# Kernel tuning notes

Measured on AMD Instinct MI355X. Metric: run time of the kernel, lower is better.

Reference implementation:

```python
import jax, jax.numpy as jnp
import numpy as np
from jax import lax

H, MEM, AUX = 1024, 256, 16
S = MEM + AUX          # total_slots
B, T = 8, 4096
TOPK = 8               # top_k_binding
GAMMA, BETA, PTS = 0.92, 0.08, 0.4  # gamma, beta, prediction_torque_scale
RANK = 10              # coupling_rank == prediction_rank


def _inv_softplus(v):
    return float(np.log(np.expm1(max(float(v), 1e-6))))


def setup_inputs() -> dict:
    key = jax.random.key(0)
    ks = jax.random.split(key, 8)
    x = jax.random.normal(ks[0], (B, T, H), dtype=jnp.float32)
    # base basis: orthonormal columns in the first MEM slots (memory_dim < hidden_dim -> QR branch)
    q, _ = jnp.linalg.qr(jax.random.normal(ks[1], (H, MEM), dtype=jnp.float32))
    basis = jnp.zeros((H, S), jnp.float32).at[:, :MEM].set(q)
    return dict(
        x=x,
        basis=basis,
        tape_init_re=jax.random.normal(ks[2], (S,), dtype=jnp.float32) / S ** 0.5,
        tape_init_im=jax.random.normal(ks[3], (S,), dtype=jnp.float32) / S ** 0.5,
        eta_raw=jnp.asarray(_inv_softplus(0.08), jnp.float32),
        alpha=jnp.asarray(0.35, jnp.float32),
        torque_rotation=jnp.zeros((S,), jnp.float32),
        w_r=jnp.zeros((S,), jnp.float32),
        breadth_gate=jnp.zeros((S,), jnp.float32),
        epsilon_factor=jax.random.normal(ks[4], (S, RANK), dtype=jnp.float32) * 0.02,
        epsilon_scale=jnp.zeros((RANK,), jnp.float32),
        epsilon_diag=jnp.zeros((S,), jnp.float32),
        pred_factor=jax.random.normal(ks[5], (S, RANK), dtype=jnp.float32) * 0.02,
        pred_scale=jnp.zeros((RANK,), jnp.float32),
        pred_diag=jnp.zeros((S,), jnp.float32),
    )


def _forward(x, basis, tape_init_re, tape_init_im, eta_raw, alpha,
             torque_rotation, w_r, breadth_gate,
             epsilon_factor, epsilon_scale, epsilon_diag,
             pred_factor, pred_scale, pred_diag):
    active = jnp.arange(S) < MEM                      # base slots active (fixed population)
    amf = active.astype(jnp.float32)
    eta = jax.nn.softplus(eta_raw)
    # low-rank Hermitian coupling epsilon and prediction operator W_pred
    eps = (epsilon_factor * epsilon_scale) @ epsilon_factor.T + jnp.diag(epsilon_diag)
    wp = (pred_factor * pred_scale) @ pred_factor.T + jnp.diag(pred_diag)
    eps_c = eps.astype(jnp.complex64)
    wp_c = wp.astype(jnp.complex64)
    rot = jnp.exp(1j * torque_rotation.astype(jnp.complex64))  # torque phase rotation
    wr_gate = jax.nn.sigmoid(w_r)
    bg = jax.nn.sigmoid(breadth_gate)

    def renorm(tape):
        masked = tape * amf
        nrm = jnp.sqrt(jnp.maximum((jnp.abs(masked) ** 2).sum(-1, keepdims=True), 1e-16))
        return masked / nrm

    tape0 = (tape_init_re + 1j * tape_init_im) * amf   # aux slots zeroed as in _complex_tape_init
    tape0 = renorm(jnp.broadcast_to(tape0, (B, S)))

    def step(carry, x_t):
        tape, prev = carry                              # [B,S] complex64 each
        m = jnp.einsum('hs,bh->bs', basis, x_t)         # project into slot space
        mag = jnp.abs(m) * amf
        kth = lax.top_k(mag, TOPK)[0][:, -1:]           # top-k binding threshold
        inj = jnp.where((mag >= kth) & active, m, 0.0).astype(jnp.complex64)
        rotated = tape * rot
        drive = jnp.einsum('st,bt->bs', eps_c, rotated)  # coupling drive
        pred = jnp.einsum('st,bt->bs', wp_c, rotated)    # prediction torque
        new = (GAMMA * rotated + eta * drive + BETA * inj
               + PTS * 1j * pred + wr_gate * prev)
        new = renorm(new)
        y = x_t + alpha * jnp.einsum('hs,bs->bh', basis, bg * new.real)
        return (new, tape), y

    (_, _), ys = lax.scan(step, (tape0, tape0), jnp.swapaxes(x, 0, 1))
    return jnp.swapaxes(ys, 0, 1)


def reference(x, basis, tape_init_re, tape_init_im, eta_raw, alpha,
              torque_rotation, w_r, breadth_gate,
              epsilon_factor, epsilon_scale, epsilon_diag,
              pred_factor, pred_scale, pred_diag):
    return _forward(x, basis, tape_init_re, tape_init_im, eta_raw, alpha,
                    torque_rotation, w_r, breadth_gate,
                    epsilon_factor, epsilon_scale, epsilon_diag,
                    pred_factor, pred_scale, pred_diag)
```

## Files before the change

kernel.cpp:

```cpp
#include <hip/hip_runtime.h>
#include <cstdint>
#include <cstddef>

#define HD    1024
#define SLOTS 272
#define MEMS  256
#define BATCH 8
#define TT    4096
#define RR    (BATCH*TT)
#define RANKC 10

#define GAMMA 0.92f
#define BETA  0.08f
#define PTS   0.4f

typedef float f32x2 __attribute__((ext_vector_type(2)));
#define PKFMA(a, b, c) __builtin_elementwise_fma((a), (b), (c))

#define DPP_ADD(v, ctrl, rmask)                                                   \
    v += __int_as_float(__builtin_amdgcn_update_dpp(                              \
        0, __float_as_int(v), (ctrl), (rmask), 0xf, true))

__device__ __forceinline__ float wave_sum_bcast(float v)
{
    DPP_ADD(v, 0xB1,  0xf);
    DPP_ADD(v, 0x4E,  0xf);
    DPP_ADD(v, 0x141, 0xf);
    DPP_ADD(v, 0x140, 0xf);
    DPP_ADD(v, 0x142, 0xa);
    DPP_ADD(v, 0x143, 0xc);
    return __int_as_float(__builtin_amdgcn_readlane(__float_as_int(v), 63));
}

__global__ void prep_kernel(const float* __restrict__ t0re, const float* __restrict__ t0im,
                            const float* __restrict__ eta_raw,
                            const float* __restrict__ trot, const float* __restrict__ w_r,
                            const float* __restrict__ bgate,
                            const float* __restrict__ eps_scale, const float* __restrict__ pred_scale,
                            const float* __restrict__ eps_diag, const float* __restrict__ pred_diag,
                            float* __restrict__ consts, int* __restrict__ flags)
{
    __shared__ float red[MEMS];
    const int s = threadIdx.x;
    const float tr = t0re[s], ti = t0im[s];
    red[s] = tr * tr + ti * ti;
    __syncthreads();
    for (int off = 128; off > 0; off >>= 1) {
        if (s < off) red[s] += red[s + off];
        __syncthreads();
    }
    const float nrm = sqrtf(fmaxf(red[0], 1e-16f));
    const float eta = log1pf(expf(eta_raw[0]));
    const float rc = cosf(trot[s]), rs = sinf(trot[s]);
    const float c1 = GAMMA + eta * eps_diag[s];
    const float c2 = PTS * pred_diag[s];
    consts[0 * MEMS + s] = 1.0f / (1.0f + expf(-w_r[s]));
    consts[1 * MEMS + s] = 1.0f / (1.0f + expf(-bgate[s]));
    consts[2 * MEMS + s] = c1 * rc - c2 * rs;
    consts[3 * MEMS + s] = c1 * rs + c2 * rc;
    consts[4 * MEMS + s] = tr / nrm;
    consts[5 * MEMS + s] = ti / nrm;
    consts[6 * MEMS + s] = rc;
    consts[7 * MEMS + s] = rs;
    if (s == 0) {
        consts[8 * MEMS] = eta;
        int f1 = 0, f2 = 0;
        for (int k = 0; k < RANKC; ++k) {
            if (eps_scale[k]  != 0.0f) f1 = 1;
            if (pred_scale[k] != 0.0f) f2 = 1;
        }
        flags[0] = f1;
        flags[1] = f2;
    }
}

__global__ __launch_bounds__(256) void proj_kernel(const float* __restrict__ x,
                                                   const float* __restrict__ basis,
                                                   float* __restrict__ M)
{
    __shared__ float As[32][68];
    __shared__ float Bs[32][68];
    const int tid  = threadIdx.x;
    const int row0 = blockIdx.x * 64;
    const int col0 = blockIdx.y * 64;
    const int mt = tid >> 4, nt = tid & 15;
    float acc[4][4] = {};
    for (int k0 = 0; k0 < HD; k0 += 32) {
        {
            int q = tid, m = q >> 3, kq = q & 7;
            float4 a = *(const float4*)&x[(size_t)(row0 + m) * HD + k0 + kq * 4];
            As[kq * 4 + 0][m] = a.x; As[kq * 4 + 1][m] = a.y;
            As[kq * 4 + 2][m] = a.z; As[kq * 4 + 3][m] = a.w;
            q = tid + 256; m = q >> 3; kq = q & 7;
            float4 b = *(const float4*)&x[(size_t)(row0 + m) * HD + k0 + kq * 4];
            As[kq * 4 + 0][m] = b.x; As[kq * 4 + 1][m] = b.y;
            As[kq * 4 + 2][m] = b.z; As[kq * 4 + 3][m] = b.w;
            q = tid; int k = q >> 4; int nq = q & 15;
            float4 c = *(const float4*)&basis[(size_t)(k0 + k) * SLOTS + col0 + nq * 4];
            *(float4*)&Bs[k][nq * 4] = c;
            q = tid + 256; k = q >> 4; nq = q & 15;
            float4 d = *(const float4*)&basis[(size_t)(k0 + k) * SLOTS + col0 + nq * 4];
            *(float4*)&Bs[k][nq * 4] = d;
        }
        __syncthreads();
#pragma unroll
        for (int kk = 0; kk < 32; ++kk) {
            float4 a = *(const float4*)&As[kk][mt * 4];
            float4 b = *(const float4*)&Bs[kk][nt * 4];
            float av[4] = {a.x, a.y, a.z, a.w};
            float bv[4] = {b.x, b.y, b.z, b.w};
#pragma unroll
            for (int i = 0; i < 4; ++i)
#pragma unroll
                for (int j = 0; j < 4; ++j) acc[i][j] += av[i] * bv[j];
        }
        __syncthreads();
    }
#pragma unroll
    for (int i = 0; i < 4; ++i) {
        float4 o = {acc[i][0], acc[i][1], acc[i][2], acc[i][3]};
        *(float4*)&M[(size_t)(row0 + mt * 4 + i) * MEMS + col0 + nt * 4] = o;
    }
}

__global__ __launch_bounds__(64) void topk_kernel(float* __restrict__ M)
{
    const int r    = blockIdx.x;
    const int lane = threadIdx.x;
    float4 v = *(const float4*)&M[(size_t)r * MEMS + lane * 4];
    float vals[4] = {fabsf(v.x), fabsf(v.y), fabsf(v.z), fabsf(v.w)};
    float keep[4] = {vals[0], vals[1], vals[2], vals[3]};
    float kv = 0.0f;
#pragma unroll
    for (int it = 0; it < 8; ++it) {
        float lm = vals[0]; int li = 0;
#pragma unroll
        for (int j = 1; j < 4; ++j)
            if (vals[j] > lm) { lm = vals[j]; li = j; }
        float bm = lm; int bi = lane * 4 + li;
#pragma unroll
        for (int off = 1; off < 64; off <<= 1) {
            float om = __shfl_xor(bm, off);
            int   oi = __shfl_xor(bi, off);
            if (om > bm || (om == bm && oi < bi)) { bm = om; bi = oi; }
        }
        kv = bm;
        if ((bi >> 2) == lane) vals[bi & 3] = -1.0f;
    }
    float4 o;
    o.x = (keep[0] >= kv) ? BETA * v.x : 0.0f;
    o.y = (keep[1] >= kv) ? BETA * v.y : 0.0f;
    o.z = (keep[2] >= kv) ? BETA * v.z : 0.0f;
    o.w = (keep[3] >= kv) ? BETA * v.w : 0.0f;
    *(float4*)&M[(size_t)r * MEMS + lane * 4] = o;
}

__global__ __launch_bounds__(64) void scan_kernel(const float* __restrict__ M,
                                                  const float* __restrict__ consts,
                                                  const int* __restrict__ flags,
                                                  const float* __restrict__ eps_fac,
                                                  const float* __restrict__ eps_scale,
                                                  const float* __restrict__ eps_diag,
                                                  const float* __restrict__ pred_fac,
                                                  const float* __restrict__ pred_scale,
                                                  const float* __restrict__ pred_diag,
                                                  float* __restrict__ Wout)
{
    const int b    = blockIdx.x;
    const int lane = threadIdx.x;
    const int s0   = lane * 4;
    const int general = flags[0] | flags[1];
    const size_t base = (size_t)b * TT * MEMS + s0;

    if (!general) {
        f32x2 wr2[2], A2[2], B2[2], nB2[2], vr[2], vi[2], qr[2], qi[2];
        {
            const float4 w4 = *(const float4*)&consts[0 * MEMS + s0];
            const float4 a4 = *(const float4*)&consts[2 * MEMS + s0];
            const float4 b4 = *(const float4*)&consts[3 * MEMS + s0];
            const float4 r4 = *(const float4*)&consts[4 * MEMS + s0];
            const float4 i4 = *(const float4*)&consts[5 * MEMS + s0];
            wr2[0] = {w4.x, w4.y};  wr2[1] = {w4.z, w4.w};
            A2[0]  = {a4.x, a4.y};  A2[1]  = {a4.z, a4.w};
            B2[0]  = {b4.x, b4.y};  B2[1]  = {b4.z, b4.w};
            nB2[0] = {-b4.x, -b4.y}; nB2[1] = {-b4.z, -b4.w};
            vr[0]  = {r4.x, r4.y};  vr[1]  = {r4.z, r4.w};
            vi[0]  = {i4.x, i4.y};  vi[1]  = {i4.z, i4.w};
            qr[0] = vr[0]; qr[1] = vr[1];
            qi[0] = vi[0]; qi[1] = vi[1];
        }
        float4 mbuf[16];
#pragma unroll
        for (int j = 0; j < 16; ++j)
            mbuf[j] = *(const float4*)&M[base + (size_t)j * MEMS];
        for (int t0 = 0; t0 < TT; t0 += 16) {
#pragma unroll
            for (int j = 0; j < 16; ++j) {
                const int t = t0 + j;
                const float4 mc = mbuf[j];
                mbuf[j] = *(const float4*)&M[base + (size_t)(t + 16) * MEMS];
                const f32x2 m0 = {mc.x, mc.y};
                const f32x2 m1 = {mc.z, mc.w};
                const f32x2 u1r0 = PKFMA(A2[0], vr[0], PKFMA(nB2[0], vi[0], PKFMA(wr2[0], qr[0], m0)));
                const f32x2 u1i0 = PKFMA(B2[0], vr[0], PKFMA(A2[0], vi[0], wr2[0] * qi[0]));
                const f32x2 u1r1 = PKFMA(A2[1], vr[1], PKFMA(nB2[1], vi[1], PKFMA(wr2[1], qr[1], m1)));
                const f32x2 u1i1 = PKFMA(B2[1], vr[1], PKFMA(A2[1], vi[1], wr2[1] * qi[1]));
                const f32x2 ps0 = PKFMA(u1i0, u1i0, u1r0 * u1r0);
                const f32x2 ps1 = PKFMA(u1i1, u1i1, u1r1 * u1r1);
                const f32x2 pp  = ps0 + ps1;
                float ss = pp.x + pp.y;
                ss = wave_sum_bcast(ss);
                const float invn = __builtin_amdgcn_rsqf(fmaxf(ss, 1e-16f));
                const f32x2 inv2 = {invn, invn};
                const f32x2 nvr0 = u1r0 * inv2, nvi0 = u1i0 * inv2;
                const f32x2 nvr1 = u1r1 * inv2, nvi1 = u1i1 * inv2;
                const float4 wq = {nvr0.x, nvr0.y, nvr1.x, nvr1.y};
                *(float4*)&Wout[base + (size_t)t * MEMS] = wq;
                qr[0] = vr[0]; qi[0] = vi[0];
                qr[1] = vr[1]; qi[1] = vi[1];
                vr[0] = nvr0;  vi[0] = nvi0;
                vr[1] = nvr1;  vi[1] = nvi1;
            }
        }
        return;
    }

    float wr4[4], ur[4], ui[4], pr[4], pi[4];
    float rc4[4], rs4[4], ed4[4], pd4[4];
#pragma unroll
    for (int i = 0; i < 4; ++i) {
        wr4[i] = consts[0 * MEMS + s0 + i];
        ur[i]  = consts[4 * MEMS + s0 + i];
        ui[i]  = consts[5 * MEMS + s0 + i];
        pr[i] = ur[i]; pi[i] = ui[i];
        rc4[i] = consts[6 * MEMS + s0 + i];
        rs4[i] = consts[7 * MEMS + s0 + i];
        ed4[i] = eps_diag[s0 + i];
        pd4[i] = pred_diag[s0 + i];
    }
    const float eta  = consts[8 * MEMS];
    const int es_any = flags[0];
    const int ps_any = flags[1];
    float4 mbuf[4];
#pragma unroll
    for (int j = 0; j < 4; ++j)
        mbuf[j] = *(const float4*)&M[base + (size_t)j * MEMS];
    for (int t0 = 0; t0 < TT; t0 += 4) {
#pragma unroll
        for (int j = 0; j < 4; ++j) {
            const int t = t0 + j;
            const float4 mc = mbuf[j];
            mbuf[j] = *(const float4*)&M[base + (size_t)(t + 4) * MEMS];
            float rr[4], ri[4], nr[4], ni[4];
#pragma unroll
            for (int i = 0; i < 4; ++i) {
                rr[i] = ur[i] * rc4[i] - ui[i] * rs4[i];
                ri[i] = ur[i] * rs4[i] + ui[i] * rc4[i];
            }
            const float mv[4] = {mc.x, mc.y, mc.z, mc.w};
#pragma unroll
            for (int i = 0; i < 4; ++i) {
                nr[i] = GAMMA * rr[i] + wr4[i] * pr[i] + eta * ed4[i] * rr[i]
                        - PTS * pd4[i] * ri[i] + mv[i];
                ni[i] = GAMMA * ri[i] + wr4[i] * pi[i] + eta * ed4[i] * ri[i]
                        + PTS * pd4[i] * rr[i];
            }
            if (es_any) {
#pragma unroll
                for (int k = 0; k < RANKC; ++k) {
                    float u[4], prj = 0.0f, pij = 0.0f;
#pragma unroll
                    for (int i = 0; i < 4; ++i) {
                        u[i] = eps_fac[(size_t)(s0 + i) * RANKC + k];
                        prj = fmaf(u[i], rr[i], prj);
                        pij = fmaf(u[i], ri[i], pij);
                    }
                    prj = wave_sum_bcast(prj);
                    pij = wave_sum_bcast(pij);
                    const float sc = eta * eps_scale[k];
#pragma unroll
                    for (int i = 0; i < 4; ++i) {
                        nr[i] = fmaf(sc * u[i], prj, nr[i]);
                        ni[i] = fmaf(sc * u[i], pij, ni[i]);
                    }
                }
            }
            if (ps_any) {
#pragma unroll
                for (int k = 0; k < RANKC; ++k) {
                    float u[4], qrj = 0.0f, qij = 0.0f;
#pragma unroll
                    for (int i = 0; i < 4; ++i) {
                        u[i] = pred_fac[(size_t)(s0 + i) * RANKC + k];
                        qrj = fmaf(u[i], rr[i], qrj);
                        qij = fmaf(u[i], ri[i], qij);
                    }
                    qrj = wave_sum_bcast(qrj);
                    qij = wave_sum_bcast(qij);
                    const float sc = PTS * pred_scale[k];
#pragma unroll
                    for (int i = 0; i < 4; ++i) {
                        nr[i] = fmaf(-sc * u[i], qij, nr[i]);
                        ni[i] = fmaf( sc * u[i], qrj, ni[i]);
                    }
                }
            }
            float ss = 0.0f;
#pragma unroll
            for (int i = 0; i < 4; ++i) ss = fmaf(nr[i], nr[i], fmaf(ni[i], ni[i], ss));
            ss = wave_sum_bcast(ss);
            const float inv = __builtin_amdgcn_rsqf(fmaxf(ss, 1e-16f));
#pragma unroll
            for (int i = 0; i < 4; ++i) {
                pr[i] = ur[i]; pi[i] = ui[i];
                ur[i] = nr[i] * inv; ui[i] = ni[i] * inv;
            }
            const float4 wq = {ur[0], ur[1], ur[2], ur[3]};
            *(float4*)&Wout[base + (size_t)t * MEMS] = wq;
        }
    }
}

__global__ __launch_bounds__(256) void outp_kernel(const float* __restrict__ W,
                                                   const float* __restrict__ basis,
                                                   const float* __restrict__ x,
                                                   const float* __restrict__ alpha_p,
                                                   const float* __restrict__ consts,
                                                   float* __restrict__ y)
{
    __shared__ float As[32][68];
    __shared__ float Bs[32][68];
    const int tid  = threadIdx.x;
    const int row0 = blockIdx.x * 64;
    const int col0 = blockIdx.y * 64;
    const int mt = tid >> 4, nt = tid & 15;
    const float alpha = alpha_p[0];
    const float* bgc  = consts + MEMS;
    const int m0 = tid >> 3, m1 = (tid + 256) >> 3;
    const int kq0 = tid & 7;
    float acc[4][4] = {};
    for (int k0 = 0; k0 < MEMS; k0 += 32) {
        {
            const float4 bgv = *(const float4*)&bgc[k0 + kq0 * 4];
            const float bx = alpha * bgv.x, by = alpha * bgv.y;
            const float bz = alpha * bgv.z, bw = alpha * bgv.w;
            float4 a = *(const float4*)&W[(size_t)(row0 + m0) * MEMS + k0 + kq0 * 4];
            As[kq0 * 4 + 0][m0] = a.x; As[kq0 * 4 + 1][m0] = a.y;
            As[kq0 * 4 + 2][m0] = a.z; As[kq0 * 4 + 3][m0] = a.w;
            float4 b = *(const float4*)&W[(size_t)(row0 + m1) * MEMS + k0 + kq0 * 4];
            As[kq0 * 4 + 0][m1] = b.x; As[kq0 * 4 + 1][m1] = b.y;
            As[kq0 * 4 + 2][m1] = b.z; As[kq0 * 4 + 3][m1] = b.w;
            int q = tid; int n = q >> 3;
            float4 c = *(const float4*)&basis[(size_t)(col0 + n) * SLOTS + k0 + kq0 * 4];
            Bs[kq0 * 4 + 0][n] = c.x * bx; Bs[kq0 * 4 + 1][n] = c.y * by;
            Bs[kq0 * 4 + 2][n] = c.z * bz; Bs[kq0 * 4 + 3][n] = c.w * bw;
            q = tid + 256; n = q >> 3;
            float4 d = *(const float4*)&basis[(size_t)(col0 + n) * SLOTS + k0 + kq0 * 4];
            Bs[kq0 * 4 + 0][n] = d.x * bx; Bs[kq0 * 4 + 1][n] = d.y * by;
            Bs[kq0 * 4 + 2][n] = d.z * bz; Bs[kq0 * 4 + 3][n] = d.w * bw;
        }
        __syncthreads();
#pragma unroll
        for (int kk = 0; kk < 32; ++kk) {
            float4 a = *(const float4*)&As[kk][mt * 4];
            float4 b = *(const float4*)&Bs[kk][nt * 4];
            float av[4] = {a.x, a.y, a.z, a.w};
            float bv[4] = {b.x, b.y, b.z, b.w};
#pragma unroll
            for (int i = 0; i < 4; ++i)
#pragma unroll
                for (int j = 0; j < 4; ++j) acc[i][j] += av[i] * bv[j];
        }
        __syncthreads();
    }
#pragma unroll
    for (int i = 0; i < 4; ++i) {
        const size_t ro = (size_t)(row0 + mt * 4 + i) * HD + col0 + nt * 4;
        float4 xv = *(const float4*)&x[ro];
        float4 o  = {xv.x + acc[i][0], xv.y + acc[i][1],
                     xv.z + acc[i][2], xv.w + acc[i][3]};
        *(float4*)&y[ro] = o;
    }
}

extern "C" void kernel_launch(void* const* d_in, const int* in_sizes, int n_in,
                              void* d_out, int out_size, void* d_ws, size_t ws_size,
                              hipStream_t stream)
{
    const float* x          = (const float*)d_in[0];
    const float* basis      = (const float*)d_in[1];
    const float* t0re       = (const float*)d_in[2];
    const float* t0im       = (const float*)d_in[3];
    const float* eta_raw    = (const float*)d_in[4];
    const float* alpha      = (const float*)d_in[5];
    const float* trot       = (const float*)d_in[6];
    const float* w_r        = (const float*)d_in[7];
    const float* bgate      = (const float*)d_in[8];
    const float* eps_fac    = (const float*)d_in[9];
    const float* eps_scale  = (const float*)d_in[10];
    const float* eps_diag   = (const float*)d_in[11];
    const float* pred_fac   = (const float*)d_in[12];
    const float* pred_scale = (const float*)d_in[13];
    const float* pred_diag  = (const float*)d_in[14];
    float* out = (float*)d_out;

    const size_t szM = (size_t)RR * MEMS * sizeof(float);
    const size_t szW = szM;
    const size_t szC = 16384;

    char* ws = (char*)d_ws;
    float *Mbuf, *Wbuf, *cbuf;
    if (ws_size >= szM + szW + szC) {
        Mbuf = (float*)(ws);
        Wbuf = (float*)(ws + szM);
        cbuf = (float*)(ws + szM + szW);
    } else {
        Mbuf = (float*)d_out;
        Wbuf = (float*)(ws);
        cbuf = (float*)(ws + szW);
    }
    int* fbuf = (int*)(cbuf + 8 * MEMS + 16);

    prep_kernel<<<1, 256, 0, stream>>>(t0re, t0im, eta_raw, trot, w_r, bgate,
                                       eps_scale, pred_scale, eps_diag, pred_diag,
                                       cbuf, fbuf);
    proj_kernel<<<dim3(RR / 64, MEMS / 64), 256, 0, stream>>>(x, basis, Mbuf);
    topk_kernel<<<RR, 64, 0, stream>>>(Mbuf);
    scan_kernel<<<BATCH, 64, 0, stream>>>(Mbuf, cbuf, fbuf,
                                          eps_fac, eps_scale, eps_diag,
                                          pred_fac, pred_scale, pred_diag,
                                          Wbuf);
    outp_kernel<<<dim3(RR / 64, HD / 64), 256, 0, stream>>>(Wbuf, basis, x, alpha,
                                                            cbuf, out);
}
```

Before: 1.106 ms.

## Defer normalization to take the wave reduction off the scan's serial critical path

Measured after the change: 1.069 ms. -3.4%, faster.

```diff
diff --git a/kernel.cpp b/kernel.cpp
--- a/kernel.cpp
+++ b/kernel.cpp
@@ -173,21 +173,29 @@
     const size_t base = (size_t)b * TT * MEMS + s0;
 
     if (!general) {
-        f32x2 wr2[2], A2[2], B2[2], nB2[2], vr[2], vi[2], qr[2], qi[2];
+        f32x2 wrg[2], A2[2], B2[2], nB2[2];
+        f32x2 wre[2], wim[2], qre[2], qim[2];
         {
             const float4 w4 = *(const float4*)&consts[0 * MEMS + s0];
             const float4 a4 = *(const float4*)&consts[2 * MEMS + s0];
             const float4 b4 = *(const float4*)&consts[3 * MEMS + s0];
             const float4 r4 = *(const float4*)&consts[4 * MEMS + s0];
             const float4 i4 = *(const float4*)&consts[5 * MEMS + s0];
-            wr2[0] = {w4.x, w4.y};  wr2[1] = {w4.z, w4.w};
+            wrg[0] = {w4.x, w4.y};  wrg[1] = {w4.z, w4.w};
             A2[0]  = {a4.x, a4.y};  A2[1]  = {a4.z, a4.w};
             B2[0]  = {b4.x, b4.y};  B2[1]  = {b4.z, b4.w};
             nB2[0] = {-b4.x, -b4.y}; nB2[1] = {-b4.z, -b4.w};
-            vr[0]  = {r4.x, r4.y};  vr[1]  = {r4.z, r4.w};
-            vi[0]  = {i4.x, i4.y};  vi[1]  = {i4.z, i4.w};
-            qr[0] = vr[0]; qr[1] = vr[1];
-            qi[0] = vi[0]; qi[1] = vi[1];
+            wre[0] = {r4.x, r4.y};  wre[1] = {r4.z, r4.w};
+            wim[0] = {i4.x, i4.y};  wim[1] = {i4.z, i4.w};
+            qre[0] = wre[0]; qre[1] = wre[1];
+            qim[0] = wim[0]; qim[1] = wim[1];
+        }
+        float ssp;
+        {
+            const f32x2 p0 = PKFMA(wim[0], wim[0], wre[0] * wre[0]);
+            const f32x2 p1 = PKFMA(wim[1], wim[1], wre[1] * wre[1]);
+            const f32x2 pp = p0 + p1;
+            ssp = pp.x + pp.y;
         }
         float4 mbuf[16];
 #pragma unroll
@@ -199,28 +207,42 @@
                 const int t = t0 + j;
                 const float4 mc = mbuf[j];
                 mbuf[j] = *(const float4*)&M[base + (size_t)(t + 16) * MEMS];
+                const float stot = wave_sum_bcast(ssp);
+                const float icv  = __builtin_amdgcn_rsqf(fmaxf(stot, 1e-16f));
+                const f32x2 ic2  = {icv, icv};
+                const f32x2 Lr0 = PKFMA(A2[0], wre[0], nB2[0] * wim[0]);
+                const f32x2 Li0 = PKFMA(B2[0], wre[0], A2[0]  * wim[0]);
+                const f32x2 Lr1 = PKFMA(A2[1], wre[1], nB2[1] * wim[1]);
+                const f32x2 Li1 = PKFMA(B2[1], wre[1], A2[1]  * wim[1]);
                 const f32x2 m0 = {mc.x, mc.y};
                 const f32x2 m1 = {mc.z, mc.w};
-                const f32x2 u1r0 = PKFMA(A2[0], vr[0], PKFMA(nB2[0], vi[0], PKFMA(wr2[0], qr[0], m0)));
-                const f32x2 u1i0 = PKFMA(B2[0], vr[0], PKFMA(A2[0], vi[0], wr2[0] * qi[0]));
-                const f32x2 u1r1 = PKFMA(A2[1], vr[1], PKFMA(nB2[1], vi[1], PKFMA(wr2[1], qr[1], m1)));
-                const f32x2 u1i1 = PKFMA(B2[1], vr[1], PKFMA(A2[1], vi[1], wr2[1] * qi[1]));
+                const f32x2 wqr0 = PKFMA(wrg[0], qre[0], m0);
+                const f32x2 wqi0 = wrg[0] * qim[0];
+                const f32x2 wqr1 = PKFMA(wrg[1], qre[1], m1);
+                const f32x2 wqi1 = wrg[1] * qim[1];
+                const f32x2 u1r0 = PKFMA(ic2, Lr0, wqr0);
+                const f32x2 u1i0 = PKFMA(ic2, Li0, wqi0);
+                const f32x2 u1r1 = PKFMA(ic2, Lr1, wqr1);
+                const f32x2 u1i1 = PKFMA(ic2, Li1, wqi1);
                 const f32x2 ps0 = PKFMA(u1i0, u1i0, u1r0 * u1r0);
                 const f32x2 ps1 = PKFMA(u1i1, u1i1, u1r1 * u1r1);
                 const f32x2 pp  = ps0 + ps1;
-                float ss = pp.x + pp.y;
-                ss = wave_sum_bcast(ss);
-                const float invn = __builtin_amdgcn_rsqf(fmaxf(ss, 1e-16f));
-                const f32x2 inv2 = {invn, invn};
-                const f32x2 nvr0 = u1r0 * inv2, nvi0 = u1i0 * inv2;
-                const f32x2 nvr1 = u1r1 * inv2, nvi1 = u1i1 * inv2;
-                const float4 wq = {nvr0.x, nvr0.y, nvr1.x, nvr1.y};
-                *(float4*)&Wout[base + (size_t)t * MEMS] = wq;
-                qr[0] = vr[0]; qi[0] = vi[0];
-                qr[1] = vr[1]; qi[1] = vi[1];
-                vr[0] = nvr0;  vi[0] = nvi0;
-                vr[1] = nvr1;  vi[1] = nvi1;
-            }
+                const f32x2 nr0 = wre[0] * ic2, ni0 = wim[0] * ic2;
+                const f32x2 nr1 = wre[1] * ic2, ni1 = wim[1] * ic2;
+                const int tr = (t - 1) < 0 ? 0 : (t - 1);
+                const float4 wq4 = {nr0.x, nr0.y, nr1.x, nr1.y};
+                *(float4*)&Wout[base + (size_t)tr * MEMS] = wq4;
+                qre[0] = nr0;  qim[0] = ni0;  qre[1] = nr1;  qim[1] = ni1;
+                wre[0] = u1r0; wim[0] = u1i0; wre[1] = u1r1; wim[1] = u1i1;
+                ssp = pp.x + pp.y;
+            }
+        }
+        {
+            const float stot = wave_sum_bcast(ssp);
+            const float icv  = __builtin_amdgcn_rsqf(fmaxf(stot, 1e-16f));
+            const float4 wq4 = {wre[0].x * icv, wre[0].y * icv,
+                                wre[1].x * icv, wre[1].y * icv};
+            *(float4*)&Wout[base + (size_t)(TT - 1) * MEMS] = wq4;
         }
         return;
     }
```
